# Kernel optimization log

Hardware: AMD Instinct MI355X
Metric: run time of the kernel (lower is better)

Reference implementation:

```python
import jax, jax.numpy as jnp
import numpy as np

B, N, D = 4, 1024, 256
NH, P = 8, 7
K = P * P
HH, WW = 64, 64


def setup_inputs() -> dict:
    key = jax.random.key(0)
    ks = jax.random.split(key, 12)
    w = lambda i, shp: (jax.random.normal(ks[i], shp, jnp.float32) * 0.02)
    return {
        "decoder_embed": jax.random.normal(ks[0], (B, N, D), jnp.float32),
        "ref_boxes": jax.random.uniform(ks[1], (B, N, 4), jnp.float32),
        "memory": jax.random.normal(ks[2], (B, D, HH, WW), jnp.float32),
        "Wq": w(3, (D, D)), "bq": jnp.zeros((D,), jnp.float32),
        "Wk": w(4, (D, D)), "bk": jnp.zeros((D,), jnp.float32),
        "Wv": w(5, (D, D)), "bv": jnp.zeros((D,), jnp.float32),
        "Wo": w(6, (D, D)), "bo": jnp.zeros((D,), jnp.float32),
        "Woff1": w(7, (D, D)), "boff1": jnp.zeros((D,), jnp.float32),
        "Woff2": w(8, (D, 2 * K)), "boff2": jnp.zeros((2 * K,), jnp.float32),
        "sigma": jnp.float32(0.1),
    }


def reference(decoder_embed, ref_boxes, memory, Wq, bq, Wk, bk, Wv, bv,
              Wo, bo, Woff1, boff1, Woff2, boff2, sigma):
    Bb, Nn, Dm = decoder_embed.shape
    _, C, H, W = memory.shape
    nh, p = NH, P
    kk = p * p
    hd = Dm // nh

    # local grid in normalized [-1,1] coords (k,) each
    coords = jnp.linspace(-(p - 1) / 2.0, (p - 1) / 2.0, p, dtype=jnp.float32)
    gx, gy = jnp.meshgrid(coords, coords, indexing='xy')
    lx = gx.reshape(-1) * (2.0 / max(W - 1, 1))
    ly = gy.reshape(-1) * (2.0 / max(H - 1, 1))

    # queries: (B, nh, N, hd)
    q = (decoder_embed @ Wq + bq).reshape(Bb, Nn, nh, hd).transpose(0, 2, 1, 3)

    # predicted offsets: (B, N, k, 2), tanh * sigma
    h = jax.nn.relu(decoder_embed @ Woff1 + boff1)
    off = jnp.tanh(h @ Woff2 + boff2).reshape(Bb, Nn, kk, 2) * sigma

    cx = ref_boxes[..., 0] * 2.0 - 1.0
    cy = ref_boxes[..., 1] * 2.0 - 1.0
    sx = jnp.clip(cx[..., None] + lx + off[..., 0], -1.0, 1.0)  # (B,N,k)
    sy = jnp.clip(cy[..., None] + ly + off[..., 1], -1.0, 1.0)

    # bilinear sample (grid_sample, align_corners=True); coords in-bounds after clip
    x = (sx + 1.0) * 0.5 * (W - 1)
    y = (sy + 1.0) * 0.5 * (H - 1)
    x0 = jnp.floor(x); y0 = jnp.floor(y)
    fx = x - x0; fy = y - y0
    x0i = jnp.clip(x0.astype(jnp.int32), 0, W - 1)
    x1i = jnp.clip(x0i + 1, 0, W - 1)
    y0i = jnp.clip(y0.astype(jnp.int32), 0, H - 1)
    y1i = jnp.clip(y0i + 1, 0, H - 1)

    mem = memory.transpose(0, 2, 3, 1)  # (B,H,W,C)
    bidx = jnp.arange(Bb)[:, None, None]
    gather = lambda yi, xi: mem[bidx, yi, xi]  # (B,N,k,C)
    sampled = (gather(y0i, x0i) * ((1 - fx) * (1 - fy))[..., None]
               + gather(y0i, x1i) * (fx * (1 - fy))[..., None]
               + gather(y1i, x0i) * ((1 - fx) * fy)[..., None]
               + gather(y1i, x1i) * (fx * fy)[..., None])  # (B,N,k,C)

    k_all = (sampled @ Wk + bk).reshape(Bb, Nn, kk, nh, hd).transpose(0, 3, 1, 2, 4)
    v_all = (sampled @ Wv + bv).reshape(Bb, Nn, kk, nh, hd).transpose(0, 3, 1, 2, 4)

    scores = jnp.einsum('bhnd,bhnkd->bhnk', q, k_all) / jnp.sqrt(jnp.float32(hd))
    attn = jax.nn.softmax(scores, axis=-1)  # (B,nh,N,k)
    out_heads = jnp.einsum('bhnk,bhnkd->bhnd', attn, v_all)
    out = out_heads.transpose(0, 2, 1, 3).reshape(Bb, Nn, Dm) @ Wo + bo
    return out, attn
```

## Files before the change

### kernel.cpp

```cpp
#include <hip/hip_runtime.h>
#include <hip/hip_bf16.h>
#include <math.h>

#define DEV __device__ __forceinline__

typedef __attribute__((ext_vector_type(8))) short bf16x8;
typedef __attribute__((ext_vector_type(4))) float f32x4;

constexpr int BB = 4, NQ1 = 1024, DM = 256, KK = 49;
constexpr int HWP = 4096;
constexpr int NQT = 4096;

DEV float bflo(unsigned u) { return __uint_as_float(u << 16); }
DEV float bfhi(unsigned u) { return __uint_as_float(u & 0xffff0000u); }
DEV unsigned pack2(float a, float b) {
    __hip_bfloat162 h2;
    h2.x = __float2bfloat16(a);
    h2.y = __float2bfloat16(b);
    unsigned u;
    __builtin_memcpy(&u, &h2, 4);
    return u;
}
DEV ushort f2bf(float a) {
    __hip_bfloat16 h = __float2bfloat16(a);
    ushort u;
    __builtin_memcpy(&u, &h, 2);
    return u;
}

__global__ __launch_bounds__(256) void k_cast(const float* __restrict__ src,
                                              ushort* __restrict__ dst) {
    int i = (blockIdx.x * 256 + threadIdx.x) * 8;
    float4 a = *(const float4*)&src[i];
    float4 b = *(const float4*)&src[i + 4];
    uint4 pk;
    pk.x = pack2(a.x, a.y);
    pk.y = pack2(a.z, a.w);
    pk.z = pack2(b.x, b.y);
    pk.w = pack2(b.z, b.w);
    *(uint4*)&dst[i] = pk;
}

__global__ __launch_bounds__(256) void k_transpose(const float* __restrict__ src,
                                                   ushort* __restrict__ dst) {
    __shared__ float tile[32][33];
    int b = blockIdx.z;
    int c0 = blockIdx.y * 32;
    int p0 = blockIdx.x * 32;
    int tx = threadIdx.x, ty = threadIdx.y;
    const float* s = src + ((size_t)b * DM + c0) * HWP + p0;
#pragma unroll
    for (int i = 0; i < 32; i += 8) tile[ty + i][tx] = s[(size_t)(ty + i) * HWP + tx];
    __syncthreads();
    ushort* d = dst + ((size_t)b * HWP + p0) * DM + c0;
#pragma unroll
    for (int i = 0; i < 32; i += 8)
        d[(size_t)(ty + i) * DM + tx] = f2bf(tile[tx][ty + i]);
}

__global__ __launch_bounds__(256) void k_transW(const float* __restrict__ src,
                                                ushort* __restrict__ dst, int K, int N) {
    __shared__ float tile[32][33];
    int n0 = blockIdx.x * 32, k0 = blockIdx.y * 32;
    int tx = threadIdx.x, ty = threadIdx.y;
#pragma unroll
    for (int i = 0; i < 32; i += 8)
        if (k0 + ty + i < K && n0 + tx < N)
            tile[ty + i][tx] = src[(size_t)(k0 + ty + i) * N + n0 + tx];
    __syncthreads();
#pragma unroll
    for (int i = 0; i < 32; i += 8)
        if (n0 + ty + i < N && k0 + tx < K)
            dst[(size_t)(n0 + ty + i) * K + k0 + tx] = f2bf(tile[tx][ty + i]);
}

__global__ __launch_bounds__(256) void k_prep_wqk(
    const float* __restrict__ Wq, const float* __restrict__ Wk,
    const float* __restrict__ bq, ushort* __restrict__ Wqk_t,
    float* __restrict__ bqk) {
    __shared__ float wks[32];
    int hc = blockIdx.x;
    int h = hc >> 8, c = hc & 255;
    int t = threadIdx.x;
    if (t < 32) wks[t] = Wk[(size_t)c * 256 + h * 32 + t];
    __syncthreads();
    const float* wq = Wq + (size_t)t * 256 + h * 32;
    float acc = 0.f;
#pragma unroll
    for (int j = 0; j < 32; ++j) acc += wq[j] * wks[j];
    Wqk_t[(size_t)hc * 256 + t] = f2bf(acc);
    if (t == 0) {
        float bacc = 0.f;
#pragma unroll
        for (int j = 0; j < 32; ++j) bacc += bq[h * 32 + j] * wks[j];
        bqk[hc] = bacc;
    }
}

__global__ __launch_bounds__(256) void k_prep_wvo(
    const float* __restrict__ Wv, const float* __restrict__ Wo,
    const float* __restrict__ bv, const float* __restrict__ bo,
    ushort* __restrict__ Wvo_t, float* __restrict__ bvo) {
    __shared__ float wos[256];
    int e = blockIdx.x;
    int t = threadIdx.x;
    wos[t] = Wo[(size_t)t * 256 + e];
    __syncthreads();
    for (int hc = t; hc < 2048; hc += 256) {
        int h = hc >> 8, c = hc & 255;
        const float* wv = Wv + (size_t)c * 256 + h * 32;
        const float* wo = &wos[h * 32];
        float acc = 0.f;
#pragma unroll
        for (int j = 0; j < 32; ++j) acc += wv[j] * wo[j];
        Wvo_t[(size_t)e * 2048 + hc] = f2bf(acc);
    }
    if (t == 0) {
        float bacc = bo[e];
#pragma unroll 8
        for (int d = 0; d < 256; ++d) bacc += bv[d] * wos[d];
        bvo[e] = bacc;
    }
}

template <int TM, int TN, int ACT, int OUTBF>
__global__ __launch_bounds__(256) void gemm_bf16(
    const ushort* __restrict__ A, const ushort* __restrict__ Bt,
    const float* __restrict__ bias, void* __restrict__ Cout,
    int N, int K, int ldc, const float* __restrict__ sclp) {
    __shared__ ushort As[TM][32];
    __shared__ ushort Bs[TN][32];
    const int t = threadIdx.x;
    const int lane = t & 63, wid = t >> 6;
    const int wr = wid >> 1, wc = wid & 1;
    const int m0 = blockIdx.y * TM, n0 = blockIdx.x * TN;
    constexpr int FM = TM / 32, FN = TN / 32;
    f32x4 acc[FM][FN];
#pragma unroll
    for (int i = 0; i < FM; ++i)
#pragma unroll
        for (int j = 0; j < FN; ++j) acc[i][j] = (f32x4){0.f, 0.f, 0.f, 0.f};

    const int l15 = lane & 15, lkg = lane >> 4;

    for (int k0 = 0; k0 < K; k0 += 32) {
        if constexpr (TM == 128) {
            int m = t >> 1, kc = (t & 1) * 16;
            const ushort* ap = &A[(size_t)(m0 + m) * K + k0 + kc];
            *(uint4*)&As[m][kc] = *(const uint4*)ap;
            *(uint4*)&As[m][kc + 8] = *(const uint4*)(ap + 8);
        } else {
            int m = t >> 2, kc = (t & 3) * 8;
            *(uint4*)&As[m][kc] = *(const uint4*)&A[(size_t)(m0 + m) * K + k0 + kc];
        }
        {
            int nn = t >> 2, kc = (t & 3) * 8;
            uint4 v = {0u, 0u, 0u, 0u};
            if (n0 + nn < N) v = *(const uint4*)&Bt[(size_t)(n0 + nn) * K + k0 + kc];
            *(uint4*)&Bs[nn][kc] = v;
        }
        __syncthreads();
        bf16x8 af[FM], bfv[FN];
#pragma unroll
        for (int mi = 0; mi < FM; ++mi)
            af[mi] = *(const bf16x8*)&As[wr * (TM / 2) + mi * 16 + l15][lkg * 8];
#pragma unroll
        for (int ni = 0; ni < FN; ++ni)
            bfv[ni] = *(const bf16x8*)&Bs[wc * (TN / 2) + ni * 16 + l15][lkg * 8];
#pragma unroll
        for (int mi = 0; mi < FM; ++mi)
#pragma unroll
            for (int ni = 0; ni < FN; ++ni)
                acc[mi][ni] = __builtin_amdgcn_mfma_f32_16x16x32_bf16(
                    af[mi], bfv[ni], acc[mi][ni], 0, 0, 0);
        __syncthreads();
    }

    float scl = (ACT == 2) ? *sclp : 0.f;
#pragma unroll
    for (int mi = 0; mi < FM; ++mi)
#pragma unroll
        for (int ni = 0; ni < FN; ++ni) {
            int col = n0 + wc * (TN / 2) + ni * 16 + l15;
            if (col < N) {
                float bcol = bias[col];
#pragma unroll
                for (int i = 0; i < 4; ++i) {
                    int row = m0 + wr * (TM / 2) + mi * 16 + lkg * 4 + i;
                    float v = acc[mi][ni][i] + bcol;
                    if (ACT == 1) v = fmaxf(v, 0.f);
                    else if (ACT == 2) v = tanhf(v) * scl;
                    if (OUTBF)
                        ((ushort*)Cout)[(size_t)row * ldc + col] = f2bf(v);
                    else
                        ((float*)Cout)[(size_t)row * ldc + col] = v;
                }
            }
        }
}

__global__ __launch_bounds__(256) void k2_attn(
    const ushort* __restrict__ memT, const float* __restrict__ refb,
    const float* __restrict__ OFFb, const float* __restrict__ QKb,
    ushort* __restrict__ AGG, float* __restrict__ attnOut) {
    __shared__ unsigned samp[49 * 132];
    __shared__ float attnL[49][8];
    const int t = threadIdx.x;
    const int wid = t >> 6, lane = t & 63;
    const int qu = __builtin_amdgcn_readfirstlane((int)((blockIdx.x & 7) * 512 + (blockIdx.x >> 3)));
    const int b = qu >> 10, n = qu & 1023;
    const bool act = lane < KK;

    const float cx = refb[(size_t)qu * 4 + 0] * 2.f - 1.f;
    const float cy = refb[(size_t)qu * 4 + 1] * 2.f - 1.f;
    float ox = 0.f, oy = 0.f;
    if (act) {
        float2 o2 = *(const float2*)&OFFb[(size_t)qu * 98 + 2 * lane];
        ox = o2.x;
        oy = o2.y;
    }
    float sx = fminf(fmaxf(cx + (float)((lane % 7) - 3) * (2.f / 63.f) + ox, -1.f), 1.f);
    float sy = fminf(fmaxf(cy + (float)(((lane / 7) % 7) - 3) * (2.f / 63.f) + oy, -1.f), 1.f);
    float xf = (sx + 1.f) * 31.5f, yf = (sy + 1.f) * 31.5f;
    float x0f = floorf(xf), y0f = floorf(yf);
    float fx = xf - x0f, fy = yf - y0f;
    int x0 = min(max((int)x0f, 0), 63), y0 = min(max((int)y0f, 0), 63);
    int x1 = min(x0 + 1, 63), y1 = min(y0 + 1, 63);
    float w00 = (1.f - fx) * (1.f - fy), w01 = fx * (1.f - fy);
    float w10 = (1.f - fx) * fy, w11 = fx * fy;

    const ushort* mb = memT + (size_t)b * HWP * DM;

    if (act) {
        const ushort* p00 = mb + (size_t)(y0 * 64 + x0) * DM + wid * 64;
        const ushort* p01 = mb + (size_t)(y0 * 64 + x1) * DM + wid * 64;
        const ushort* p10 = mb + (size_t)(y1 * 64 + x0) * DM + wid * 64;
        const ushort* p11 = mb + (size_t)(y1 * 64 + x1) * DM + wid * 64;
        unsigned* srow = &samp[lane * 132 + wid * 32];
#pragma unroll
        for (int cc = 0; cc < 64; cc += 8) {
            uint4 u00 = *(const uint4*)(p00 + cc);
            uint4 u01 = *(const uint4*)(p01 + cc);
            uint4 u10 = *(const uint4*)(p10 + cc);
            uint4 u11 = *(const uint4*)(p11 + cc);
            const unsigned* a00 = (const unsigned*)&u00;
            const unsigned* a01 = (const unsigned*)&u01;
            const unsigned* a10 = (const unsigned*)&u10;
            const unsigned* a11 = (const unsigned*)&u11;
            float s[8];
#pragma unroll
            for (int q = 0; q < 4; ++q) {
                s[2 * q] = w00 * bflo(a00[q]) + w01 * bflo(a01[q]) +
                           w10 * bflo(a10[q]) + w11 * bflo(a11[q]);
                s[2 * q + 1] = w00 * bfhi(a00[q]) + w01 * bfhi(a01[q]) +
                               w10 * bfhi(a10[q]) + w11 * bfhi(a11[q]);
            }
            uint4 pk;
            pk.x = pack2(s[0], s[1]);
            pk.y = pack2(s[2], s[3]);
            pk.z = pack2(s[4], s[5]);
            pk.w = pack2(s[6], s[7]);
            *(uint4*)&srow[cc / 2] = pk;
        }
    }
    __syncthreads();

    const int qkoff = __builtin_amdgcn_readfirstlane(qu * 2048 + wid * 512);
    const float* qk0 = QKb + qkoff;
    float p0 = 0.f, p1 = 0.f;
    if (act) {
        const unsigned* srow = &samp[lane * 132];
#pragma unroll 8
        for (int cc = 0; cc < 256; cc += 8) {
            uint4 u = *(const uint4*)&srow[cc / 2];
            const unsigned* au = (const unsigned*)&u;
            float s[8];
#pragma unroll
            for (int q = 0; q < 4; ++q) {
                s[2 * q] = bflo(au[q]);
                s[2 * q + 1] = bfhi(au[q]);
            }
            float4 qa = *(const float4*)(qk0 + cc);
            float4 qb = *(const float4*)(qk0 + cc + 4);
            float4 qc = *(const float4*)(qk0 + 256 + cc);
            float4 qd = *(const float4*)(qk0 + 256 + cc + 4);
            p0 += s[0] * qa.x + s[1] * qa.y + s[2] * qa.z + s[3] * qa.w +
                  s[4] * qb.x + s[5] * qb.y + s[6] * qb.z + s[7] * qb.w;
            p1 += s[0] * qc.x + s[1] * qc.y + s[2] * qc.z + s[3] * qc.w +
                  s[4] * qd.x + s[5] * qd.y + s[6] * qd.z + s[7] * qd.w;
        }
    }
    const float scl = 0.17677669529663687f;
    float s0 = act ? p0 * scl : -INFINITY;
    float s1 = act ? p1 * scl : -INFINITY;
    float m0v = s0, m1v = s1;
#pragma unroll
    for (int off = 32; off; off >>= 1) {
        m0v = fmaxf(m0v, __shfl_xor(m0v, off));
        m1v = fmaxf(m1v, __shfl_xor(m1v, off));
    }
    float e0 = act ? __expf(s0 - m0v) : 0.f;
    float e1 = act ? __expf(s1 - m1v) : 0.f;
    float sum0 = e0, sum1 = e1;
#pragma unroll
    for (int off = 32; off; off >>= 1) {
        sum0 += __shfl_xor(sum0, off);
        sum1 += __shfl_xor(sum1, off);
    }
    float at0 = e0 / sum0, at1 = e1 / sum1;
    if (act) {
        attnL[lane][2 * wid] = at0;
        attnL[lane][2 * wid + 1] = at1;
        attnOut[((size_t)(b * 8 + 2 * wid) * 1024 + n) * 49 + lane] = at0;
        attnOut[((size_t)(b * 8 + 2 * wid + 1) * 1024 + n) * 49 + lane] = at1;
    }
    __syncthreads();

    const int c = t;
    float acc[8];
#pragma unroll
    for (int h = 0; h < 8; ++h) acc[h] = 0.f;
#pragma unroll 7
    for (int k = 0; k < KK; ++k) {
        unsigned d = samp[k * 132 + (c >> 1)];
        float sv = (c & 1) ? bfhi(d) : bflo(d);
        float4 a0 = *(const float4*)&attnL[k][0];
        float4 a1 = *(const float4*)&attnL[k][4];
        acc[0] += a0.x * sv;
        acc[1] += a0.y * sv;
        acc[2] += a0.z * sv;
        acc[3] += a0.w * sv;
        acc[4] += a1.x * sv;
        acc[5] += a1.y * sv;
        acc[6] += a1.z * sv;
        acc[7] += a1.w * sv;
    }
    ushort* ag = AGG + (size_t)qu * 2048 + c;
#pragma unroll
    for (int h = 0; h < 8; ++h) ag[h * 256] = f2bf(acc[h]);
}

extern "C" void kernel_launch(void* const* d_in, const int* in_sizes, int n_in,
                              void* d_out, int out_size, void* d_ws, size_t ws_size,
                              hipStream_t stream) {
    (void)in_sizes; (void)n_in; (void)out_size; (void)ws_size;
    const float* X     = (const float*)d_in[0];
    const float* refb  = (const float*)d_in[1];
    const float* mem   = (const float*)d_in[2];
    const float* Wq    = (const float*)d_in[3];
    const float* bq    = (const float*)d_in[4];
    const float* Wk    = (const float*)d_in[5];
    const float* Wv    = (const float*)d_in[7];
    const float* bv    = (const float*)d_in[8];
    const float* Wo    = (const float*)d_in[9];
    const float* bo    = (const float*)d_in[10];
    const float* Woff1 = (const float*)d_in[11];
    const float* boff1 = (const float*)d_in[12];
    const float* Woff2 = (const float*)d_in[13];
    const float* boff2 = (const float*)d_in[14];
    const float* sigma = (const float*)d_in[15];

    float* out  = (float*)d_out;
    float* attn = out + (size_t)NQT * DM;

    float* ws = (float*)d_ws;
    ushort* memT  = (ushort*)(ws + 0);
    ushort* Xbf   = (ushort*)(ws + 2097152);
    ushort* WqkT  = (ushort*)(ws + 2621440);
    float*  bqk   = ws + 2883584;
    ushort* WvoT  = (ushort*)(ws + 2885632);
    float*  bvo   = ws + 3147776;
    ushort* W1t   = (ushort*)(ws + 3148032);
    ushort* W2t   = (ushort*)(ws + 3180800);
    float*  QKb   = ws + 3193344;
    ushort* Hbf   = (ushort*)(ws + 11581952);
    float*  OFFb  = ws + 11844096;
    ushort* AGGb  = (ushort*)(ws + 12245504);

    k_cast<<<512, 256, 0, stream>>>(X, Xbf);
    k_transpose<<<dim3(128, 8, 4), dim3(32, 8), 0, stream>>>(mem, memT);
    k_prep_wqk<<<2048, 256, 0, stream>>>(Wq, Wk, bq, WqkT, bqk);
    k_prep_wvo<<<256, 256, 0, stream>>>(Wv, Wo, bv, bo, WvoT, bvo);
    k_transW<<<dim3(8, 8), dim3(32, 8), 0, stream>>>(Woff1, W1t, 256, 256);
    k_transW<<<dim3(4, 8), dim3(32, 8), 0, stream>>>(Woff2, W2t, 256, 98);

    gemm_bf16<128, 64, 0, 0><<<dim3(32, 32), 256, 0, stream>>>(
        Xbf, WqkT, bqk, QKb, 2048, 256, 2048, nullptr);
    gemm_bf16<64, 64, 1, 1><<<dim3(4, 64), 256, 0, stream>>>(
        Xbf, W1t, boff1, Hbf, 256, 256, 256, nullptr);
    gemm_bf16<64, 64, 2, 0><<<dim3(2, 64), 256, 0, stream>>>(
        Hbf, W2t, boff2, OFFb, 98, 256, 98, sigma);

    k2_attn<<<4096, 256, 0, stream>>>(memT, refb, OFFb, QKb, AGGb, attn);

    gemm_bf16<64, 64, 0, 0><<<dim3(4, 64), 256, 0, stream>>>(
        AGGb, WvoT, bvo, out, 256, 2048, 256, nullptr);
}
```

Before: 268.2 us.

## Merge prep kernels, swizzle GEMM LDS, fuse QK dot into sampling

Folds the six preprocessing launches into one kernel that dispatches on block index, cutting launch overhead. The GEMM gains a BK template parameter and an XOR-swizzled LDS layout to reduce bank conflicts, and the final GEMM uses BK=64. In the attention kernel each wave computes partial per-head dot products right after bilinear sampling of its channel quarter, then reduces them through a small shared buffer instead of rereading all sampled channels. The partial sums are rounded to bf16 in that buffer, which adds some precision loss, and keeping eight accumulators plus the query-key loads raises register pressure.

```diff
diff --git a/kernel.cpp b/kernel.cpp
--- a/kernel.cpp
+++ b/kernel.cpp
@@ -28,113 +28,114 @@
     return u;
 }
 
-__global__ __launch_bounds__(256) void k_cast(const float* __restrict__ src,
-                                              ushort* __restrict__ dst) {
-    int i = (blockIdx.x * 256 + threadIdx.x) * 8;
-    float4 a = *(const float4*)&src[i];
-    float4 b = *(const float4*)&src[i + 4];
-    uint4 pk;
-    pk.x = pack2(a.x, a.y);
-    pk.y = pack2(a.z, a.w);
-    pk.z = pack2(b.x, b.y);
-    pk.w = pack2(b.z, b.w);
-    *(uint4*)&dst[i] = pk;
-}
-
-__global__ __launch_bounds__(256) void k_transpose(const float* __restrict__ src,
-                                                   ushort* __restrict__ dst) {
-    __shared__ float tile[32][33];
-    int b = blockIdx.z;
-    int c0 = blockIdx.y * 32;
-    int p0 = blockIdx.x * 32;
-    int tx = threadIdx.x, ty = threadIdx.y;
-    const float* s = src + ((size_t)b * DM + c0) * HWP + p0;
-#pragma unroll
-    for (int i = 0; i < 32; i += 8) tile[ty + i][tx] = s[(size_t)(ty + i) * HWP + tx];
-    __syncthreads();
-    ushort* d = dst + ((size_t)b * HWP + p0) * DM + c0;
-#pragma unroll
-    for (int i = 0; i < 32; i += 8)
-        d[(size_t)(ty + i) * DM + tx] = f2bf(tile[tx][ty + i]);
-}
-
-__global__ __launch_bounds__(256) void k_transW(const float* __restrict__ src,
-                                                ushort* __restrict__ dst, int K, int N) {
-    __shared__ float tile[32][33];
-    int n0 = blockIdx.x * 32, k0 = blockIdx.y * 32;
-    int tx = threadIdx.x, ty = threadIdx.y;
-#pragma unroll
-    for (int i = 0; i < 32; i += 8)
-        if (k0 + ty + i < K && n0 + tx < N)
-            tile[ty + i][tx] = src[(size_t)(k0 + ty + i) * N + n0 + tx];
-    __syncthreads();
-#pragma unroll
-    for (int i = 0; i < 32; i += 8)
-        if (n0 + ty + i < N && k0 + tx < K)
-            dst[(size_t)(n0 + ty + i) * K + k0 + tx] = f2bf(tile[tx][ty + i]);
-}
-
-__global__ __launch_bounds__(256) void k_prep_wqk(
+__global__ __launch_bounds__(256) void k_prep(
+    const float* __restrict__ X, ushort* __restrict__ Xbf,
+    const float* __restrict__ mem, ushort* __restrict__ memT,
     const float* __restrict__ Wq, const float* __restrict__ Wk,
-    const float* __restrict__ bq, ushort* __restrict__ Wqk_t,
-    float* __restrict__ bqk) {
-    __shared__ float wks[32];
-    int hc = blockIdx.x;
-    int h = hc >> 8, c = hc & 255;
-    int t = threadIdx.x;
-    if (t < 32) wks[t] = Wk[(size_t)c * 256 + h * 32 + t];
-    __syncthreads();
-    const float* wq = Wq + (size_t)t * 256 + h * 32;
-    float acc = 0.f;
-#pragma unroll
-    for (int j = 0; j < 32; ++j) acc += wq[j] * wks[j];
-    Wqk_t[(size_t)hc * 256 + t] = f2bf(acc);
-    if (t == 0) {
-        float bacc = 0.f;
-#pragma unroll
-        for (int j = 0; j < 32; ++j) bacc += bq[h * 32 + j] * wks[j];
-        bqk[hc] = bacc;
-    }
-}
-
-__global__ __launch_bounds__(256) void k_prep_wvo(
+    const float* __restrict__ bq, ushort* __restrict__ WqkT, float* __restrict__ bqk,
     const float* __restrict__ Wv, const float* __restrict__ Wo,
     const float* __restrict__ bv, const float* __restrict__ bo,
-    ushort* __restrict__ Wvo_t, float* __restrict__ bvo) {
-    __shared__ float wos[256];
-    int e = blockIdx.x;
-    int t = threadIdx.x;
-    wos[t] = Wo[(size_t)t * 256 + e];
-    __syncthreads();
-    for (int hc = t; hc < 2048; hc += 256) {
+    ushort* __restrict__ WvoT, float* __restrict__ bvo,
+    const float* __restrict__ Woff1, ushort* __restrict__ W1t,
+    const float* __restrict__ Woff2, ushort* __restrict__ W2t) {
+    __shared__ float smem[32 * 33];
+    const int blk = blockIdx.x;
+    const int t = threadIdx.x;
+
+    if (blk < 512) {
+        int i = (blk * 256 + t) * 8;
+        float4 a = *(const float4*)&X[i];
+        float4 b = *(const float4*)&X[i + 4];
+        uint4 pk;
+        pk.x = pack2(a.x, a.y);
+        pk.y = pack2(a.z, a.w);
+        pk.z = pack2(b.x, b.y);
+        pk.w = pack2(b.z, b.w);
+        *(uint4*)&Xbf[i] = pk;
+    } else if (blk < 4608) {
+        int r = blk - 512;
+        int p0 = (r & 127) * 32;
+        int c0 = ((r >> 7) & 7) * 32;
+        int b = r >> 10;
+        int tx = t & 31, ty = t >> 5;
+        float (*tile)[33] = (float(*)[33])smem;
+        const float* s = mem + ((size_t)b * DM + c0) * HWP + p0;
+#pragma unroll
+        for (int i = 0; i < 32; i += 8) tile[ty + i][tx] = s[(size_t)(ty + i) * HWP + tx];
+        __syncthreads();
+        ushort* d = memT + ((size_t)b * HWP + p0) * DM + c0;
+#pragma unroll
+        for (int i = 0; i < 32; i += 8)
+            d[(size_t)(ty + i) * DM + tx] = f2bf(tile[tx][ty + i]);
+    } else if (blk < 6656) {
+        int hc = blk - 4608;
         int h = hc >> 8, c = hc & 255;
-        const float* wv = Wv + (size_t)c * 256 + h * 32;
-        const float* wo = &wos[h * 32];
+        if (t < 32) smem[t] = Wk[(size_t)c * 256 + h * 32 + t];
+        __syncthreads();
+        const float* wq = Wq + (size_t)t * 256 + h * 32;
         float acc = 0.f;
 #pragma unroll
-        for (int j = 0; j < 32; ++j) acc += wv[j] * wo[j];
-        Wvo_t[(size_t)e * 2048 + hc] = f2bf(acc);
-    }
-    if (t == 0) {
-        float bacc = bo[e];
+        for (int j = 0; j < 32; ++j) acc += wq[j] * smem[j];
+        WqkT[(size_t)hc * 256 + t] = f2bf(acc);
+        if (t == 0) {
+            float bacc = 0.f;
+#pragma unroll
+            for (int j = 0; j < 32; ++j) bacc += bq[h * 32 + j] * smem[j];
+            bqk[hc] = bacc;
+        }
+    } else if (blk < 6912) {
+        int e = blk - 6656;
+        smem[t] = Wo[(size_t)t * 256 + e];
+        __syncthreads();
+        for (int hc = t; hc < 2048; hc += 256) {
+            int h = hc >> 8, c = hc & 255;
+            const float* wv = Wv + (size_t)c * 256 + h * 32;
+            const float* wo = &smem[h * 32];
+            float acc = 0.f;
+#pragma unroll
+            for (int j = 0; j < 32; ++j) acc += wv[j] * wo[j];
+            WvoT[(size_t)e * 2048 + hc] = f2bf(acc);
+        }
+        if (t == 0) {
+            float bacc = bo[e];
 #pragma unroll 8
-        for (int d = 0; d < 256; ++d) bacc += bv[d] * wos[d];
-        bvo[e] = bacc;
-    }
-}
-
-template <int TM, int TN, int ACT, int OUTBF>
+            for (int d = 0; d < 256; ++d) bacc += bv[d] * smem[d];
+            bvo[e] = bacc;
+        }
+    } else {
+        const float* src;
+        ushort* dst;
+        int K = 256, N, r;
+        if (blk < 6976) { r = blk - 6912; src = Woff1; dst = W1t; N = 256; }
+        else            { r = blk - 6976; src = Woff2; dst = W2t; N = 98; }
+        int nblk = (N + 31) / 32;
+        int n0 = (r % nblk) * 32, k0 = (r / nblk) * 32;
+        int tx = t & 31, ty = t >> 5;
+        float (*tile)[33] = (float(*)[33])smem;
+#pragma unroll
+        for (int i = 0; i < 32; i += 8)
+            if (n0 + tx < N) tile[ty + i][tx] = src[(size_t)(k0 + ty + i) * N + n0 + tx];
+        __syncthreads();
+#pragma unroll
+        for (int i = 0; i < 32; i += 8)
+            if (n0 + ty + i < N)
+                dst[(size_t)(n0 + ty + i) * K + k0 + tx] = f2bf(tile[tx][ty + i]);
+    }
+}
+
+template <int TM, int TN, int BK, int ACT, int OUTBF>
 __global__ __launch_bounds__(256) void gemm_bf16(
     const ushort* __restrict__ A, const ushort* __restrict__ Bt,
     const float* __restrict__ bias, void* __restrict__ Cout,
     int N, int K, int ldc, const float* __restrict__ sclp) {
-    __shared__ ushort As[TM][32];
-    __shared__ ushort Bs[TN][32];
+    constexpr int SL = BK / 8;
+    __shared__ ushort As[TM][BK];
+    __shared__ ushort Bs[TN][BK];
     const int t = threadIdx.x;
     const int lane = t & 63, wid = t >> 6;
     const int wr = wid >> 1, wc = wid & 1;
     const int m0 = blockIdx.y * TM, n0 = blockIdx.x * TN;
-    constexpr int FM = TM / 32, FN = TN / 32;
+    constexpr int FM = TM / 32, FN = TN / 32, KS = BK / 32;
     f32x4 acc[FM][FN];
 #pragma unroll
     for (int i = 0; i < FM; ++i)
@@ -143,36 +144,48 @@
 
     const int l15 = lane & 15, lkg = lane >> 4;
 
-    for (int k0 = 0; k0 < K; k0 += 32) {
-        if constexpr (TM == 128) {
-            int m = t >> 1, kc = (t & 1) * 16;
-            const ushort* ap = &A[(size_t)(m0 + m) * K + k0 + kc];
-            *(uint4*)&As[m][kc] = *(const uint4*)ap;
-            *(uint4*)&As[m][kc + 8] = *(const uint4*)(ap + 8);
-        } else {
-            int m = t >> 2, kc = (t & 3) * 8;
-            *(uint4*)&As[m][kc] = *(const uint4*)&A[(size_t)(m0 + m) * K + k0 + kc];
-        }
-        {
-            int nn = t >> 2, kc = (t & 3) * 8;
+    for (int k0 = 0; k0 < K; k0 += BK) {
+        constexpr int NA = TM * SL / 256;
+#pragma unroll
+        for (int i = 0; i < NA; ++i) {
+            int idx = t + i * 256;
+            int m = idx / SL, sl = idx % SL;
+            int ss = sl ^ ((m >> 1) & (SL - 1));
+            *(uint4*)&As[m][ss * 8] = *(const uint4*)&A[(size_t)(m0 + m) * K + k0 + sl * 8];
+        }
+        constexpr int NB = TN * SL / 256;
+#pragma unroll
+        for (int i = 0; i < NB; ++i) {
+            int idx = t + i * 256;
+            int nn = idx / SL, sl = idx % SL;
+            int ss = sl ^ ((nn >> 1) & (SL - 1));
             uint4 v = {0u, 0u, 0u, 0u};
-            if (n0 + nn < N) v = *(const uint4*)&Bt[(size_t)(n0 + nn) * K + k0 + kc];
-            *(uint4*)&Bs[nn][kc] = v;
-        }
-        __syncthreads();
-        bf16x8 af[FM], bfv[FN];
-#pragma unroll
-        for (int mi = 0; mi < FM; ++mi)
-            af[mi] = *(const bf16x8*)&As[wr * (TM / 2) + mi * 16 + l15][lkg * 8];
-#pragma unroll
-        for (int ni = 0; ni < FN; ++ni)
-            bfv[ni] = *(const bf16x8*)&Bs[wc * (TN / 2) + ni * 16 + l15][lkg * 8];
-#pragma unroll
-        for (int mi = 0; mi < FM; ++mi)
-#pragma unroll
-            for (int ni = 0; ni < FN; ++ni)
-                acc[mi][ni] = __builtin_amdgcn_mfma_f32_16x16x32_bf16(
-                    af[mi], bfv[ni], acc[mi][ni], 0, 0, 0);
+            if (n0 + nn < N) v = *(const uint4*)&Bt[(size_t)(n0 + nn) * K + k0 + sl * 8];
+            *(uint4*)&Bs[nn][ss * 8] = v;
+        }
+        __syncthreads();
+#pragma unroll
+        for (int ks = 0; ks < KS; ++ks) {
+            bf16x8 af[FM], bfv[FN];
+#pragma unroll
+            for (int mi = 0; mi < FM; ++mi) {
+                int R = wr * (TM / 2) + mi * 16 + l15;
+                int ss = (lkg + ks * 4) ^ ((R >> 1) & (SL - 1));
+                af[mi] = *(const bf16x8*)&As[R][ss * 8];
+            }
+#pragma unroll
+            for (int ni = 0; ni < FN; ++ni) {
+                int R = wc * (TN / 2) + ni * 16 + l15;
+                int ss = (lkg + ks * 4) ^ ((R >> 1) & (SL - 1));
+                bfv[ni] = *(const bf16x8*)&Bs[R][ss * 8];
+            }
+#pragma unroll
+            for (int mi = 0; mi < FM; ++mi)
+#pragma unroll
+                for (int ni = 0; ni < FN; ++ni)
+                    acc[mi][ni] = __builtin_amdgcn_mfma_f32_16x16x32_bf16(
+                        af[mi], bfv[ni], acc[mi][ni], 0, 0, 0);
+        }
         __syncthreads();
     }
 
@@ -204,6 +217,7 @@
     const float* __restrict__ OFFb, const float* __restrict__ QKb,
     ushort* __restrict__ AGG, float* __restrict__ attnOut) {
     __shared__ unsigned samp[49 * 132];
+    __shared__ unsigned pxb[4][4][64];
     __shared__ float attnL[49][8];
     const int t = threadIdx.x;
     const int wid = t >> 6, lane = t & 63;
@@ -230,6 +244,11 @@
     float w10 = (1.f - fx) * fy, w11 = fx * fy;
 
     const ushort* mb = memT + (size_t)b * HWP * DM;
+    const float* qk0 = QKb + (size_t)__builtin_amdgcn_readfirstlane(qu * 2048 + wid * 64);
+
+    float p[8];
+#pragma unroll
+    for (int h = 0; h < 8; ++h) p[h] = 0.f;
 
     if (act) {
         const ushort* p00 = mb + (size_t)(y0 * 64 + x0) * DM + wid * 64;
@@ -237,7 +256,7 @@
         const ushort* p10 = mb + (size_t)(y1 * 64 + x0) * DM + wid * 64;
         const ushort* p11 = mb + (size_t)(y1 * 64 + x1) * DM + wid * 64;
         unsigned* srow = &samp[lane * 132 + wid * 32];
-#pragma unroll
+#pragma unroll 2
         for (int cc = 0; cc < 64; cc += 8) {
             uint4 u00 = *(const uint4*)(p00 + cc);
             uint4 u01 = *(const uint4*)(p01 + cc);
@@ -261,33 +280,27 @@
             pk.z = pack2(s[4], s[5]);
             pk.w = pack2(s[6], s[7]);
             *(uint4*)&srow[cc / 2] = pk;
-        }
+#pragma unroll
+            for (int h = 0; h < 8; ++h) {
+                float4 qa = *(const float4*)(qk0 + h * 256 + cc);
+                float4 qb = *(const float4*)(qk0 + h * 256 + cc + 4);
+                p[h] += s[0] * qa.x + s[1] * qa.y + s[2] * qa.z + s[3] * qa.w +
+                        s[4] * qb.x + s[5] * qb.y + s[6] * qb.z + s[7] * qb.w;
+            }
+        }
+#pragma unroll
+        for (int hp = 0; hp < 4; ++hp)
+            pxb[wid][hp][lane] = pack2(p[2 * hp], p[2 * hp + 1]);
     }
     __syncthreads();
 
-    const int qkoff = __builtin_amdgcn_readfirstlane(qu * 2048 + wid * 512);
-    const float* qk0 = QKb + qkoff;
     float p0 = 0.f, p1 = 0.f;
     if (act) {
-        const unsigned* srow = &samp[lane * 132];
-#pragma unroll 8
-        for (int cc = 0; cc < 256; cc += 8) {
-            uint4 u = *(const uint4*)&srow[cc / 2];
-            const unsigned* au = (const unsigned*)&u;
-            float s[8];
-#pragma unroll
-            for (int q = 0; q < 4; ++q) {
-                s[2 * q] = bflo(au[q]);
-                s[2 * q + 1] = bfhi(au[q]);
-            }
-            float4 qa = *(const float4*)(qk0 + cc);
-            float4 qb = *(const float4*)(qk0 + cc + 4);
-            float4 qc = *(const float4*)(qk0 + 256 + cc);
-            float4 qd = *(const float4*)(qk0 + 256 + cc + 4);
-            p0 += s[0] * qa.x + s[1] * qa.y + s[2] * qa.z + s[3] * qa.w +
-                  s[4] * qb.x + s[5] * qb.y + s[6] * qb.z + s[7] * qb.w;
-            p1 += s[0] * qc.x + s[1] * qc.y + s[2] * qc.z + s[3] * qc.w +
-                  s[4] * qd.x + s[5] * qd.y + s[6] * qd.z + s[7] * qd.w;
+#pragma unroll
+        for (int w = 0; w < 4; ++w) {
+            unsigned u = pxb[w][wid][lane];
+            p0 += bflo(u);
+            p1 += bfhi(u);
         }
     }
     const float scl = 0.17677669529663687f;
@@ -377,22 +390,18 @@
     float*  OFFb  = ws + 11844096;
     ushort* AGGb  = (ushort*)(ws + 12245504);
 
-    k_cast<<<512, 256, 0, stream>>>(X, Xbf);
-    k_transpose<<<dim3(128, 8, 4), dim3(32, 8), 0, stream>>>(mem, memT);
-    k_prep_wqk<<<2048, 256, 0, stream>>>(Wq, Wk, bq, WqkT, bqk);
-    k_prep_wvo<<<256, 256, 0, stream>>>(Wv, Wo, bv, bo, WvoT, bvo);
-    k_transW<<<dim3(8, 8), dim3(32, 8), 0, stream>>>(Woff1, W1t, 256, 256);
-    k_transW<<<dim3(4, 8), dim3(32, 8), 0, stream>>>(Woff2, W2t, 256, 98);
-
-    gemm_bf16<128, 64, 0, 0><<<dim3(32, 32), 256, 0, stream>>>(
+    k_prep<<<7008, 256, 0, stream>>>(X, Xbf, mem, memT, Wq, Wk, bq, WqkT, bqk,
+                                     Wv, Wo, bv, bo, WvoT, bvo, Woff1, W1t, Woff2, W2t);
+
+    gemm_bf16<128, 64, 32, 0, 0><<<dim3(32, 32), 256, 0, stream>>>(
         Xbf, WqkT, bqk, QKb, 2048, 256, 2048, nullptr);
-    gemm_bf16<64, 64, 1, 1><<<dim3(4, 64), 256, 0, stream>>>(
+    gemm_bf16<64, 64, 32, 1, 1><<<dim3(4, 64), 256, 0, stream>>>(
         Xbf, W1t, boff1, Hbf, 256, 256, 256, nullptr);
-    gemm_bf16<64, 64, 2, 0><<<dim3(2, 64), 256, 0, stream>>>(
+    gemm_bf16<64, 64, 32, 2, 0><<<dim3(2, 64), 256, 0, stream>>>(
         Hbf, W2t, boff2, OFFb, 98, 256, 98, sigma);
 
     k2_attn<<<4096, 256, 0, stream>>>(memT, refb, OFFb, QKb, AGGb, attn);
 
-    gemm_bf16<64, 64, 0, 0><<<dim3(4, 64), 256, 0, stream>>>(
+    gemm_bf16<64, 64, 64, 0, 0><<<dim3(4, 64), 256, 0, stream>>>(
         AGGb, WvoT, bvo, out, 256, 2048, 256, nullptr);
 }
```

After: 255.0 us. -4.9%, faster.
